# Performance work log

Hardware: AMD Instinct MI355X
Metric: run time of the kernel (lower is better)

Reference implementation:

```python
import jax, jax.numpy as jnp
import numpy as np

DIM = 1024
NUM_HEADS = 16
HEAD_DIM = DIM // NUM_HEADS
EPS = 1e-5


def setup_inputs() -> dict:
    key = jax.random.key(0)
    ks = jax.random.split(key, 5)
    B, N = 2, 2048
    x = jax.random.normal(ks[0], (B, N, DIM), dtype=jnp.float32)
    # nn.Linear(dim, 3*dim): weight [3*dim, dim], bias [3*dim]
    w_qkv = jax.random.normal(ks[1], (3 * DIM, DIM), dtype=jnp.float32) * (DIM ** -0.5)
    b_qkv = jnp.zeros((3 * DIM,), dtype=jnp.float32)
    # qk-norm LayerNorm(head_dim) affine params
    q_gamma = jnp.ones((HEAD_DIM,), dtype=jnp.float32)
    q_beta = jnp.zeros((HEAD_DIM,), dtype=jnp.float32)
    k_gamma = jnp.ones((HEAD_DIM,), dtype=jnp.float32)
    k_beta = jnp.zeros((HEAD_DIM,), dtype=jnp.float32)
    # output projection nn.Linear(dim, dim)
    w_proj = jax.random.normal(ks[2], (DIM, DIM), dtype=jnp.float32) * (DIM ** -0.5)
    b_proj = jnp.zeros((DIM,), dtype=jnp.float32)
    return {
        "x": x,
        "w_qkv": w_qkv, "b_qkv": b_qkv,
        "q_gamma": q_gamma, "q_beta": q_beta,
        "k_gamma": k_gamma, "k_beta": k_beta,
        "w_proj": w_proj, "b_proj": b_proj,
    }


def _layernorm(t, gamma, beta):
    # LayerNorm over last dim (head_dim)
    mu = jnp.mean(t, axis=-1, keepdims=True)
    var = jnp.mean(jnp.square(t - mu), axis=-1, keepdims=True)
    return (t - mu) * jax.lax.rsqrt(var + EPS) * gamma + beta


def reference(x, w_qkv, b_qkv, q_gamma, q_beta, k_gamma, k_beta, w_proj, b_proj):
    B, N, C = x.shape
    H, D = NUM_HEADS, HEAD_DIM
    scale = D ** -0.5
    # QKV projection: [B,N,3C] -> [3,B,H,N,D]
    qkv = x @ w_qkv.T + b_qkv
    qkv = qkv.reshape(B, N, 3, H, D).transpose(2, 0, 3, 1, 4)
    q, k, v = qkv[0], qkv[1], qkv[2]
    # per-head qk-norm
    q = _layernorm(q, q_gamma, q_beta)
    k = _layernorm(k, k_gamma, k_beta)
    # scaled dot-product attention
    scores = jnp.einsum("bhqd,bhkd->bhqk", q, k) * scale
    attn = jax.nn.softmax(scores, axis=-1)
    out = jnp.einsum("bhqk,bhkd->bhqd", attn, v)  # [B,H,N,D]
    out = out.transpose(0, 2, 1, 3).reshape(B, N, C)
    # output projection
    return out @ w_proj.T + b_proj
```

## Files before the change

kernel.cpp:

```cpp
#include <hip/hip_runtime.h>

typedef _Float16 half8 __attribute__((ext_vector_type(8)));
typedef _Float16 half4 __attribute__((ext_vector_type(4)));
typedef float f32x4 __attribute__((ext_vector_type(4)));
typedef float f32x16 __attribute__((ext_vector_type(16)));
typedef unsigned int uint;
typedef uint uint4v __attribute__((ext_vector_type(4)));

#define MFMA16(a, b, c) __builtin_amdgcn_mfma_f32_16x16x32_f16((a), (b), (c), 0, 0, 0)
#define MFMA32(a, b, c) __builtin_amdgcn_mfma_f32_32x32x16_f16((a), (b), (c), 0, 0, 0)

#define GLOAD16(g, l)                                            \
    __builtin_amdgcn_global_load_lds(                            \
        (const __attribute__((address_space(1))) void*)(g),      \
        (__attribute__((address_space(3))) void*)(l), 16, 0, 0)


__global__ __launch_bounds__(256) void cvt_all(const float* __restrict__ x,
                                               const float* __restrict__ wq,
                                               const float* __restrict__ wp,
                                               _Float16* __restrict__ xh,
                                               _Float16* __restrict__ wqh,
                                               _Float16* __restrict__ wph) {
    int i = blockIdx.x * 256 + threadIdx.x;
    const float* src;
    _Float16* dst;
    int off;
    if (i < 524288) { src = x; dst = xh; off = i; }
    else if (i < 917504) { src = wq; dst = wqh; off = i - 524288; }
    else { src = wp; dst = wph; off = i - 917504; }
    const float4* p = reinterpret_cast<const float4*>(src) + 2 * (size_t)off;
    float4 a = p[0], b = p[1];
    half8 o;
    o[0] = (_Float16)a.x; o[1] = (_Float16)a.y; o[2] = (_Float16)a.z; o[3] = (_Float16)a.w;
    o[4] = (_Float16)b.x; o[5] = (_Float16)b.y; o[6] = (_Float16)b.z; o[7] = (_Float16)b.w;
    reinterpret_cast<half8*>(dst)[off] = o;
}

template <int EPI>
__global__ __launch_bounds__(256) void gemm_nt(const _Float16* __restrict__ A,
                                               const _Float16* __restrict__ W,
                                               const float* __restrict__ bias,
                                               void* __restrict__ Cout, int K,
                                               const float* __restrict__ qg,
                                               const float* __restrict__ qb,
                                               const float* __restrict__ kg,
                                               const float* __restrict__ kb) {
    __shared__ __align__(16) _Float16 Al[128 * 64];
    __shared__ __align__(16) _Float16 Wl[128 * 64];
    const int tid = threadIdx.x, l = tid & 63, w = tid >> 6;
    const int lin = blockIdx.x + (blockIdx.y << 5);
    const int nwg = gridDim.x * gridDim.y;
    const int wg = (lin & 7) * (nwg >> 3) + (lin >> 3);
    const int bm = (wg & 31) * 128, bn = (wg >> 5) * 128;
    const int wr = (w >> 1) * 64, wc = (w & 1) * 64;
    const int srow = l >> 3;
    const int schunk = (l & 7) ^ srow;

    f32x4 acc[4][4] = {};
    const _Float16* Ag = A + (size_t)(bm + 32 * w + srow) * K + 8 * schunk;
    const _Float16* Wg = W + (size_t)(bn + 32 * w + srow) * K + 8 * schunk;
    const int rswz = (l & 7) << 3;

    for (int kt = 0; kt < K; kt += 64) {
        __syncthreads();
#pragma unroll
        for (int t = 0; t < 4; t++) {
            GLOAD16(Ag + (size_t)(8 * t) * K + kt, &Al[(32 * w + 8 * t) * 64]);
            GLOAD16(Wg + (size_t)(8 * t) * K + kt, &Wl[(32 * w + 8 * t) * 64]);
        }
        __syncthreads();
#pragma unroll
        for (int ks = 0; ks < 2; ks++) {
            const int koff = (ks * 32 + (l >> 4) * 8) ^ rswz;
            half8 af[4], wf[4];
#pragma unroll
            for (int t = 0; t < 4; t++) {
                af[t] = *(const half8*)&Al[(wr + t * 16 + (l & 15)) * 64 + koff];
                wf[t] = *(const half8*)&Wl[(wc + t * 16 + (l & 15)) * 64 + koff];
            }
            __builtin_amdgcn_s_setprio(1);
#pragma unroll
            for (int mt = 0; mt < 4; mt++)
#pragma unroll
                for (int nt = 0; nt < 4; nt++)
                    acc[mt][nt] = MFMA16(af[mt], wf[nt], acc[mt][nt]);
            __builtin_amdgcn_s_setprio(0);
        }
    }

    if (EPI == 0) {
        const int ncol = bn + wc;
        const int s = ncol >> 10;
        const int hh = (ncol >> 6) & 15;
        const float* gam = (s == 0) ? qg : kg;
        const float* bet = (s == 0) ? qb : kb;
        float ga[4], be[4];
        if (s < 2) {
#pragma unroll
            for (int nt = 0; nt < 4; nt++) {
                int d = nt * 16 + (l & 15);
                ga[nt] = gam[d];
                be[nt] = bet[d];
            }
        }
        const float cs = (s == 0) ? 0.18033688f : 1.f;
#pragma unroll
        for (int mt = 0; mt < 4; mt++)
#pragma unroll
            for (int r = 0; r < 4; r++) {
                float v[4];
                float sm = 0.f, s2 = 0.f;
#pragma unroll
                for (int nt = 0; nt < 4; nt++) {
                    v[nt] = acc[mt][nt][r] + bias[ncol + nt * 16 + (l & 15)];
                    sm += v[nt];
                    s2 += v[nt] * v[nt];
                }
                int m = bm + wr + mt * 16 + (l >> 4) * 4 + r;
                int b = m >> 11, nn = m & 2047;
                _Float16* dst = (_Float16*)Cout +
                    (size_t)((((s * 2 + b) * 16 + hh) * 2048 + nn) << 6);
                if (s < 2) {
#pragma unroll
                    for (int off = 1; off < 16; off <<= 1) {
                        sm += __shfl_xor(sm, off);
                        s2 += __shfl_xor(s2, off);
                    }
                    float mean = sm * (1.f / 64.f);
                    float var = s2 * (1.f / 64.f) - mean * mean;
                    float rs = rsqrtf(var + 1e-5f) * cs;
#pragma unroll
                    for (int nt = 0; nt < 4; nt++) {
                        int d = nt * 16 + (l & 15);
                        dst[d] = (_Float16)((v[nt] - mean) * rs * ga[nt] + be[nt] * cs);
                    }
                } else {
#pragma unroll
                    for (int nt = 0; nt < 4; nt++)
                        dst[nt * 16 + (l & 15)] = (_Float16)v[nt];
                }
            }
    } else {
#pragma unroll
        for (int mt = 0; mt < 4; mt++)
#pragma unroll
            for (int nt = 0; nt < 4; nt++)
#pragma unroll
                for (int r = 0; r < 4; r++) {
                    int m = bm + wr + mt * 16 + (l >> 4) * 4 + r;
                    int n = bn + wc + nt * 16 + (l & 15);
                    ((float*)Cout)[(size_t)m * 1024 + n] = acc[mt][nt][r] + bias[n];
                }
    }
}

__global__ __launch_bounds__(256) void attn_kernel(const _Float16* __restrict__ qkv,
                                                   _Float16* __restrict__ out) {
    const int tid = threadIdx.x;
    const int l = tid & 63, w = tid >> 6;
    const int l31 = l & 31, hi = l >> 5;
    const int bid = blockIdx.x;
    const int wg = (bid & 7) * 64 + (bid >> 3);
    const int head = wg >> 4, qt = wg & 15;
    const int b = head >> 4, h = head & 15;
    const size_t hstride = (size_t)2048 * 64;
    const _Float16* Q = qkv + (size_t)((0 + b) * 16 + h) * hstride;
    const _Float16* Kp = qkv + (size_t)((2 + b) * 16 + h) * hstride;
    const _Float16* Vp = qkv + (size_t)((4 + b) * 16 + h) * hstride;

    __shared__ __align__(16) _Float16 Kl[2][64 * 64];
    __shared__ __align__(16) _Float16 Vt[2][64 * 64];

    const int r0q = qt * 128 + w * 32;
    half8 qf[4];
    {
        const _Float16* Qrow = Q + (size_t)(r0q + l31) * 64 + 8 * hi;
#pragma unroll
        for (int dk = 0; dk < 4; dk++) qf[dk] = *(const half8*)&Qrow[16 * dk];
    }

    const int srow = l >> 3, sch = l & 7;
    auto stageK = [&](int it, _Float16* dst) {
#pragma unroll
        for (int t = 0; t < 2; t++) {
            int r0 = 16 * w + 8 * t;
            const _Float16* g = Kp + (size_t)(it * 64 + r0 + srow) * 64 + 8 * (sch ^ srow);
            GLOAD16(g, &dst[r0 * 64]);
        }
    };
    auto loadV = [&](int it, half8& v0, half8& v1) {
        const _Float16* g = Vp + (size_t)(it * 64 + 16 * w + srow) * 64 + 8 * sch;
        v0 = *(const half8*)g;
        v1 = *(const half8*)(g + 8 * 64);
    };
    auto scatterV = [&](half8 v0, half8 v1, _Float16* dst) {
        const int j0 = 16 * w + srow;
        const int d0 = 8 * sch;
#pragma unroll
        for (int i = 0; i < 8; i++) {
            const int sw = (i ^ sch) << 3;
            dst[(d0 + i) * 64 + (j0 ^ sw)] = v0[i];
            dst[(d0 + i) * 64 + ((j0 + 8) ^ sw)] = v1[i];
        }
    };

    float lrun = 0.f;
    f32x16 o0 = {}, o1 = {};

    half8 va, vb;
    stageK(0, Kl[0]);
    loadV(0, va, vb);
    scatterV(va, vb, Vt[0]);
    __syncthreads();

    const int kswz = (l31 & 7) << 3;
    const int vswz0 = ((l31 & 7) ^ (l31 >> 3)) << 3;
    const int vswz1 = vswz0 ^ (4 << 3);

    for (int it = 0; it < 32; ++it) {
        const int cur = it & 1;
        const _Float16* Kc = Kl[cur];
        const _Float16* Vc = Vt[cur];
        if (it + 1 < 32) {
            stageK(it + 1, Kl[cur ^ 1]);
            loadV(it + 1, va, vb);
        }
        f32x16 st0 = {}, st1 = {};
#pragma unroll
        for (int dk = 0; dk < 4; dk++) {
            const int colr = 16 * dk + 8 * hi;
            half8 kf0 = *(const half8*)&Kc[l31 * 64 + (colr ^ kswz)];
            half8 kf1 = *(const half8*)&Kc[(32 + l31) * 64 + (colr ^ kswz)];
            __builtin_amdgcn_s_setprio(1);
            st0 = MFMA32(kf0, qf[dk], st0);
            st1 = MFMA32(kf1, qf[dk], st1);
            __builtin_amdgcn_s_setprio(0);
        }
        float lh = 0.f;
#pragma unroll
        for (int r = 0; r < 16; r++) { st0[r] = exp2f(st0[r]); lh += st0[r]; }
#pragma unroll
        for (int r = 0; r < 16; r++) { st1[r] = exp2f(st1[r]); lh += st1[r]; }
        lrun += lh;

#define PV_CHUNK(stv, c)                                                                   \
        {                                                                                  \
            uint pk0 = __builtin_bit_cast(uint, __builtin_amdgcn_cvt_pkrtz(stv[(c & 1) * 8 + 0], stv[(c & 1) * 8 + 1])); \
            uint pk1 = __builtin_bit_cast(uint, __builtin_amdgcn_cvt_pkrtz(stv[(c & 1) * 8 + 2], stv[(c & 1) * 8 + 3])); \
            uint pk2 = __builtin_bit_cast(uint, __builtin_amdgcn_cvt_pkrtz(stv[(c & 1) * 8 + 4], stv[(c & 1) * 8 + 5])); \
            uint pk3 = __builtin_bit_cast(uint, __builtin_amdgcn_cvt_pkrtz(stv[(c & 1) * 8 + 6], stv[(c & 1) * 8 + 7])); \
            uint sa = __shfl_xor(pk0, 32), sb = __shfl_xor(pk1, 32);                       \
            uint sc = __shfl_xor(pk2, 32), sd = __shfl_xor(pk3, 32);                       \
            uint4v fu = {hi ? sc : pk0, hi ? sd : pk1, hi ? pk2 : sa, hi ? pk3 : sb};      \
            half8 pfrag = __builtin_bit_cast(half8, fu);                                   \
            const int colc = 16 * (c) + 8 * hi;                                            \
            half8 vf0 = *(const half8*)&Vc[l31 * 64 + (colc ^ vswz0)];                     \
            half8 vf1 = *(const half8*)&Vc[(32 + l31) * 64 + (colc ^ vswz1)];              \
            __builtin_amdgcn_s_setprio(1);                                                 \
            o0 = MFMA32(vf0, pfrag, o0);                                                   \
            o1 = MFMA32(vf1, pfrag, o1);                                                   \
            __builtin_amdgcn_s_setprio(0);                                                 \
        }
        PV_CHUNK(st0, 0)
        PV_CHUNK(st0, 1)
        PV_CHUNK(st1, 2)
        PV_CHUNK(st1, 3)
#undef PV_CHUNK

        if (it + 1 < 32) scatterV(va, vb, Vt[cur ^ 1]);
        __syncthreads();
    }

    lrun += __shfl_xor(lrun, 32);
    const float inv = __builtin_amdgcn_rcpf(lrun);
    const int tok = r0q + l31;
    _Float16* orow = out + (size_t)(b * 2048 + tok) * 1024 + h * 64;
#pragma unroll
    for (int g = 0; g < 4; g++) {
        half4 h4a, h4b;
#pragma unroll
        for (int j = 0; j < 4; j++) {
            h4a[j] = (_Float16)(o0[4 * g + j] * inv);
            h4b[j] = (_Float16)(o1[4 * g + j] * inv);
        }
        *(half4*)&orow[8 * g + 4 * hi] = h4a;
        *(half4*)&orow[32 + 8 * g + 4 * hi] = h4b;
    }
}

extern "C" void kernel_launch(void* const* d_in, const int* in_sizes, int n_in,
                              void* d_out, int out_size, void* d_ws, size_t ws_size,
                              hipStream_t stream) {
    const float* x = (const float*)d_in[0];
    const float* w_qkv = (const float*)d_in[1];
    const float* b_qkv = (const float*)d_in[2];
    const float* q_gamma = (const float*)d_in[3];
    const float* q_beta = (const float*)d_in[4];
    const float* k_gamma = (const float*)d_in[5];
    const float* k_beta = (const float*)d_in[6];
    const float* w_proj = (const float*)d_in[7];
    const float* b_proj = (const float*)d_in[8];

    char* ws = (char*)d_ws;
    _Float16* xh = (_Float16*)(ws + 0);
    _Float16* wqkvh = (_Float16*)(ws + 8388608);
    _Float16* wprojh = (_Float16*)(ws + 14680064);
    _Float16* qkvh = (_Float16*)(ws + 16777216);
    _Float16* attnh = (_Float16*)(ws + 41943040);

    cvt_all<<<4096, 256, 0, stream>>>(x, w_qkv, w_proj, xh, wqkvh, wprojh);

    gemm_nt<0><<<dim3(32, 24), 256, 0, stream>>>(xh, wqkvh, b_qkv, (void*)qkvh, 1024,
                                                 q_gamma, q_beta, k_gamma, k_beta);

    attn_kernel<<<512, 256, 0, stream>>>(qkvh, attnh);

    gemm_nt<1><<<dim3(32, 8), 256, 0, stream>>>(attnh, wprojh, b_proj, d_out, 1024,
                                                nullptr, nullptr, nullptr, nullptr);
}
```

Measured before the change: 223.3 us.

## Split attention over key quarters, double-buffer narrower GEMM tiles, use permlane32 swap

```diff
diff --git a/kernel.cpp b/kernel.cpp
--- a/kernel.cpp
+++ b/kernel.cpp
@@ -5,6 +5,7 @@
 typedef float f32x4 __attribute__((ext_vector_type(4)));
 typedef float f32x16 __attribute__((ext_vector_type(16)));
 typedef unsigned int uint;
+typedef uint uint2v __attribute__((ext_vector_type(2)));
 typedef uint uint4v __attribute__((ext_vector_type(4)));
 
 #define MFMA16(a, b, c) __builtin_amdgcn_mfma_f32_16x16x32_f16((a), (b), (c), 0, 0, 0)
@@ -37,7 +38,7 @@
     reinterpret_cast<half8*>(dst)[off] = o;
 }
 
-template <int EPI>
+template <int MT, int EPI>
 __global__ __launch_bounds__(256) void gemm_nt(const _Float16* __restrict__ A,
                                                const _Float16* __restrict__ W,
                                                const float* __restrict__ bias,
@@ -46,47 +47,58 @@
                                                const float* __restrict__ qb,
                                                const float* __restrict__ kg,
                                                const float* __restrict__ kb) {
-    __shared__ __align__(16) _Float16 Al[128 * 64];
-    __shared__ __align__(16) _Float16 Wl[128 * 64];
+    constexpr int TM = MT * 32;
+    __shared__ __align__(16) _Float16 Al[2][TM * 64];
+    __shared__ __align__(16) _Float16 Wl[2][128 * 64];
     const int tid = threadIdx.x, l = tid & 63, w = tid >> 6;
-    const int lin = blockIdx.x + (blockIdx.y << 5);
+    const int lin = blockIdx.x + (blockIdx.y << 6);
     const int nwg = gridDim.x * gridDim.y;
     const int wg = (lin & 7) * (nwg >> 3) + (lin >> 3);
-    const int bm = (wg & 31) * 128, bn = (wg >> 5) * 128;
-    const int wr = (w >> 1) * 64, wc = (w & 1) * 64;
+    const int bm = (wg & 63) * TM, bn = (wg >> 6) * 128;
+    const int wr = (w >> 1) * (MT * 16), wc = (w & 1) * 64;
     const int srow = l >> 3;
     const int schunk = (l & 7) ^ srow;
 
-    f32x4 acc[4][4] = {};
-    const _Float16* Ag = A + (size_t)(bm + 32 * w + srow) * K + 8 * schunk;
+    const _Float16* Ag = A + (size_t)(bm + (TM / 4) * w + srow) * K + 8 * schunk;
     const _Float16* Wg = W + (size_t)(bn + 32 * w + srow) * K + 8 * schunk;
     const int rswz = (l & 7) << 3;
-
-    for (int kt = 0; kt < K; kt += 64) {
-        __syncthreads();
-#pragma unroll
-        for (int t = 0; t < 4; t++) {
-            GLOAD16(Ag + (size_t)(8 * t) * K + kt, &Al[(32 * w + 8 * t) * 64]);
-            GLOAD16(Wg + (size_t)(8 * t) * K + kt, &Wl[(32 * w + 8 * t) * 64]);
-        }
-        __syncthreads();
+    const int nk = K >> 6;
+
+    auto stage = [&](int t, int buf) {
+        const int kt = t << 6;
+#pragma unroll
+        for (int i = 0; i < MT; i++)
+            GLOAD16(Ag + (size_t)(8 * i) * K + kt, &Al[buf][((TM / 4) * w + 8 * i) * 64]);
+#pragma unroll
+        for (int i = 0; i < 4; i++)
+            GLOAD16(Wg + (size_t)(8 * i) * K + kt, &Wl[buf][(32 * w + 8 * i) * 64]);
+    };
+
+    f32x4 acc[MT][4] = {};
+    stage(0, 0);
+    __syncthreads();
+    for (int t = 0; t < nk; ++t) {
+        const int cur = t & 1;
+        if (t + 1 < nk) stage(t + 1, cur ^ 1);
 #pragma unroll
         for (int ks = 0; ks < 2; ks++) {
             const int koff = (ks * 32 + (l >> 4) * 8) ^ rswz;
-            half8 af[4], wf[4];
-#pragma unroll
-            for (int t = 0; t < 4; t++) {
-                af[t] = *(const half8*)&Al[(wr + t * 16 + (l & 15)) * 64 + koff];
-                wf[t] = *(const half8*)&Wl[(wc + t * 16 + (l & 15)) * 64 + koff];
-            }
+            half8 af[MT], wf[4];
+#pragma unroll
+            for (int i = 0; i < MT; i++)
+                af[i] = *(const half8*)&Al[cur][(wr + i * 16 + (l & 15)) * 64 + koff];
+#pragma unroll
+            for (int i = 0; i < 4; i++)
+                wf[i] = *(const half8*)&Wl[cur][(wc + i * 16 + (l & 15)) * 64 + koff];
             __builtin_amdgcn_s_setprio(1);
 #pragma unroll
-            for (int mt = 0; mt < 4; mt++)
+            for (int mt = 0; mt < MT; mt++)
 #pragma unroll
                 for (int nt = 0; nt < 4; nt++)
                     acc[mt][nt] = MFMA16(af[mt], wf[nt], acc[mt][nt]);
             __builtin_amdgcn_s_setprio(0);
         }
+        __syncthreads();
     }
 
     if (EPI == 0) {
@@ -106,7 +118,7 @@
         }
         const float cs = (s == 0) ? 0.18033688f : 1.f;
 #pragma unroll
-        for (int mt = 0; mt < 4; mt++)
+        for (int mt = 0; mt < MT; mt++)
 #pragma unroll
             for (int r = 0; r < 4; r++) {
                 float v[4];
@@ -143,7 +155,7 @@
             }
     } else {
 #pragma unroll
-        for (int mt = 0; mt < 4; mt++)
+        for (int mt = 0; mt < MT; mt++)
 #pragma unroll
             for (int nt = 0; nt < 4; nt++)
 #pragma unroll
@@ -155,19 +167,25 @@
     }
 }
 
+template <int SPLIT>
 __global__ __launch_bounds__(256) void attn_kernel(const _Float16* __restrict__ qkv,
-                                                   _Float16* __restrict__ out) {
+                                                   _Float16* __restrict__ out,
+                                                   float* __restrict__ lpart) {
     const int tid = threadIdx.x;
     const int l = tid & 63, w = tid >> 6;
     const int l31 = l & 31, hi = l >> 5;
     const int bid = blockIdx.x;
-    const int wg = (bid & 7) * 64 + (bid >> 3);
-    const int head = wg >> 4, qt = wg & 15;
+    const int nwg = 512 * SPLIT;
+    const int wg = (bid & 7) * (nwg >> 3) + (bid >> 3);
+    int head, qt, quarter;
+    if (SPLIT == 4) { head = wg >> 6; qt = (wg >> 2) & 15; quarter = wg & 3; }
+    else            { head = wg >> 4; qt = wg & 15;        quarter = 0; }
     const int b = head >> 4, h = head & 15;
     const size_t hstride = (size_t)2048 * 64;
     const _Float16* Q = qkv + (size_t)((0 + b) * 16 + h) * hstride;
-    const _Float16* Kp = qkv + (size_t)((2 + b) * 16 + h) * hstride;
-    const _Float16* Vp = qkv + (size_t)((4 + b) * 16 + h) * hstride;
+    const _Float16* Kp = qkv + (size_t)((2 + b) * 16 + h) * hstride + (size_t)quarter * 512 * 64;
+    const _Float16* Vp = qkv + (size_t)((4 + b) * 16 + h) * hstride + (size_t)quarter * 512 * 64;
+    const int NIT = (SPLIT == 4) ? 8 : 32;
 
     __shared__ __align__(16) _Float16 Kl[2][64 * 64];
     __shared__ __align__(16) _Float16 Vt[2][64 * 64];
@@ -218,11 +236,11 @@
     const int vswz0 = ((l31 & 7) ^ (l31 >> 3)) << 3;
     const int vswz1 = vswz0 ^ (4 << 3);
 
-    for (int it = 0; it < 32; ++it) {
+    for (int it = 0; it < NIT; ++it) {
         const int cur = it & 1;
         const _Float16* Kc = Kl[cur];
         const _Float16* Vc = Vt[cur];
-        if (it + 1 < 32) {
+        if (it + 1 < NIT) {
             stageK(it + 1, Kl[cur ^ 1]);
             loadV(it + 1, va, vb);
         }
@@ -250,9 +268,9 @@
             uint pk1 = __builtin_bit_cast(uint, __builtin_amdgcn_cvt_pkrtz(stv[(c & 1) * 8 + 2], stv[(c & 1) * 8 + 3])); \
             uint pk2 = __builtin_bit_cast(uint, __builtin_amdgcn_cvt_pkrtz(stv[(c & 1) * 8 + 4], stv[(c & 1) * 8 + 5])); \
             uint pk3 = __builtin_bit_cast(uint, __builtin_amdgcn_cvt_pkrtz(stv[(c & 1) * 8 + 6], stv[(c & 1) * 8 + 7])); \
-            uint sa = __shfl_xor(pk0, 32), sb = __shfl_xor(pk1, 32);                       \
-            uint sc = __shfl_xor(pk2, 32), sd = __shfl_xor(pk3, 32);                       \
-            uint4v fu = {hi ? sc : pk0, hi ? sd : pk1, hi ? pk2 : sa, hi ? pk3 : sb};      \
+            uint2v s02 = __builtin_amdgcn_permlane32_swap(pk0, pk2, false, false);         \
+            uint2v s13 = __builtin_amdgcn_permlane32_swap(pk1, pk3, false, false);         \
+            uint4v fu = {s02.x, s13.x, s02.y, s13.y};                                      \
             half8 pfrag = __builtin_bit_cast(half8, fu);                                   \
             const int colc = 16 * (c) + 8 * hi;                                            \
             half8 vf0 = *(const half8*)&Vc[l31 * 64 + (colc ^ vswz0)];                     \
@@ -268,25 +286,65 @@
         PV_CHUNK(st1, 3)
 #undef PV_CHUNK
 
-        if (it + 1 < 32) scatterV(va, vb, Vt[cur ^ 1]);
+        if (it + 1 < NIT) scatterV(va, vb, Vt[cur ^ 1]);
         __syncthreads();
     }
 
     lrun += __shfl_xor(lrun, 32);
-    const float inv = __builtin_amdgcn_rcpf(lrun);
     const int tok = r0q + l31;
-    _Float16* orow = out + (size_t)(b * 2048 + tok) * 1024 + h * 64;
-#pragma unroll
-    for (int g = 0; g < 4; g++) {
-        half4 h4a, h4b;
-#pragma unroll
-        for (int j = 0; j < 4; j++) {
-            h4a[j] = (_Float16)(o0[4 * g + j] * inv);
-            h4b[j] = (_Float16)(o1[4 * g + j] * inv);
-        }
-        *(half4*)&orow[8 * g + 4 * hi] = h4a;
-        *(half4*)&orow[32 + 8 * g + 4 * hi] = h4b;
-    }
+    if (SPLIT == 4) {
+        _Float16* orow = out + (size_t)quarter * 4194304 + (size_t)(b * 2048 + tok) * 1024 + h * 64;
+#pragma unroll
+        for (int g = 0; g < 4; g++) {
+            half4 h4a, h4b;
+#pragma unroll
+            for (int j = 0; j < 4; j++) {
+                h4a[j] = (_Float16)o0[4 * g + j];
+                h4b[j] = (_Float16)o1[4 * g + j];
+            }
+            *(half4*)&orow[8 * g + 4 * hi] = h4a;
+            *(half4*)&orow[32 + 8 * g + 4 * hi] = h4b;
+        }
+        if (!hi) lpart[quarter * 65536 + (b * 16 + h) * 2048 + tok] = lrun;
+    } else {
+        const float inv = __builtin_amdgcn_rcpf(lrun);
+        _Float16* orow = out + (size_t)(b * 2048 + tok) * 1024 + h * 64;
+#pragma unroll
+        for (int g = 0; g < 4; g++) {
+            half4 h4a, h4b;
+#pragma unroll
+            for (int j = 0; j < 4; j++) {
+                h4a[j] = (_Float16)(o0[4 * g + j] * inv);
+                h4b[j] = (_Float16)(o1[4 * g + j] * inv);
+            }
+            *(half4*)&orow[8 * g + 4 * hi] = h4a;
+            *(half4*)&orow[32 + 8 * g + 4 * hi] = h4b;
+        }
+    }
+}
+
+__global__ __launch_bounds__(256) void merge_attn(const _Float16* __restrict__ onum,
+                                                  const float* __restrict__ lpart,
+                                                  _Float16* __restrict__ attnh) {
+    const int i = blockIdx.x * 256 + threadIdx.x;
+    const int tokb = i >> 7;
+    const int c0 = (i & 127) * 8;
+    const int h = c0 >> 6;
+    const int bb = tokb >> 11, tok = tokb & 2047;
+    const int li = (bb * 16 + h) * 2048 + tok;
+    float lt = lpart[li] + lpart[65536 + li] + lpart[131072 + li] + lpart[196608 + li];
+    float inv = __builtin_amdgcn_rcpf(lt);
+    float acc[8] = {};
+#pragma unroll
+    for (int q = 0; q < 4; q++) {
+        half8 v = *(const half8*)&onum[(size_t)q * 4194304 + (size_t)tokb * 1024 + c0];
+#pragma unroll
+        for (int j = 0; j < 8; j++) acc[j] += (float)v[j];
+    }
+    half8 o;
+#pragma unroll
+    for (int j = 0; j < 8; j++) o[j] = (_Float16)(acc[j] * inv);
+    *(half8*)&attnh[(size_t)tokb * 1024 + c0] = o;
 }
 
 extern "C" void kernel_launch(void* const* d_in, const int* in_sizes, int n_in,
@@ -308,14 +366,22 @@
     _Float16* wprojh = (_Float16*)(ws + 14680064);
     _Float16* qkvh = (_Float16*)(ws + 16777216);
     _Float16* attnh = (_Float16*)(ws + 41943040);
+    _Float16* onum = (_Float16*)(ws + 50331648);
+    float* lp = (float*)(ws + 83886080);
+    const bool split = ws_size >= 84934656;
 
     cvt_all<<<4096, 256, 0, stream>>>(x, w_qkv, w_proj, xh, wqkvh, wprojh);
 
-    gemm_nt<0><<<dim3(32, 24), 256, 0, stream>>>(xh, wqkvh, b_qkv, (void*)qkvh, 1024,
-                                                 q_gamma, q_beta, k_gamma, k_beta);
-
-    attn_kernel<<<512, 256, 0, stream>>>(qkvh, attnh);
-
-    gemm_nt<1><<<dim3(32, 8), 256, 0, stream>>>(attnh, wprojh, b_proj, d_out, 1024,
-                                                nullptr, nullptr, nullptr, nullptr);
-}
+    gemm_nt<2, 0><<<dim3(64, 24), 256, 0, stream>>>(xh, wqkvh, b_qkv, (void*)qkvh, 1024,
+                                                    q_gamma, q_beta, k_gamma, k_beta);
+
+    if (split) {
+        attn_kernel<4><<<2048, 256, 0, stream>>>(qkvh, onum, lp);
+        merge_attn<<<2048, 256, 0, stream>>>(onum, lp, attnh);
+    } else {
+        attn_kernel<1><<<512, 256, 0, stream>>>(qkvh, attnh, nullptr);
+    }
+
+    gemm_nt<2, 1><<<dim3(64, 8), 256, 0, stream>>>(attnh, wprojh, b_proj, d_out, 1024,
+                                                   nullptr, nullptr, nullptr, nullptr);
+}
```

Measured after the change: 231.9 us. 3.9% more time.
